# Kernel optimization log

Hardware: AMD Instinct MI355X
Metric: run time of the kernel (lower is better)

## Reference

```python
import jax, jax.numpy as jnp
import numpy as np

NUM_ANCHORS = 9  # 3 ratios * 3 sizes


def setup_inputs() -> dict:
    key = jax.random.key(0)
    k0, k1, k2, k3 = jax.random.split(key, 4)
    B, C, H, W = 4, 256, 200, 336
    resnet_features = jax.random.normal(k0, (B, C, H, W), dtype=jnp.float32)
    # 3x3 conv: C -> 512
    W1 = jax.random.normal(k1, (512, C, 3, 3), dtype=jnp.float32) * 0.02
    b1 = jnp.zeros((512,), dtype=jnp.float32)
    # 1x1 cls head: 512 -> 9*2
    Wc = jax.random.normal(k2, (NUM_ANCHORS * 2, 512), dtype=jnp.float32) * 0.02
    bc = jnp.zeros((NUM_ANCHORS * 2,), dtype=jnp.float32)
    # 1x1 bbox head: 512 -> 9*4
    Wb = jax.random.normal(k3, (NUM_ANCHORS * 4, 512), dtype=jnp.float32) * 0.02
    bb = jnp.zeros((NUM_ANCHORS * 4,), dtype=jnp.float32)
    return {"resnet_features": resnet_features, "W1": W1, "b1": b1,
            "Wc": Wc, "bc": bc, "Wb": Wb, "bb": bb}


def reference(resnet_features, W1, b1, Wc, bc, Wb, bb):
    B = resnet_features.shape[0]
    # conv3x3 + ReLU (padding=1 -> SAME)
    feat = jax.lax.conv_general_dilated(
        resnet_features, W1, window_strides=(1, 1), padding='SAME',
        dimension_numbers=('NCHW', 'OIHW', 'NCHW'))
    feat = jax.nn.relu(feat + b1[None, :, None, None])  # [B,512,H,W]
    # 1x1 conv heads as channel contractions
    cls = jnp.einsum('bchw,oc->bohw', feat, Wc) + bc[None, :, None, None]
    box = jnp.einsum('bchw,oc->bohw', feat, Wb) + bb[None, :, None, None]
    # permute(0,2,3,1).view(B,-1,2/4)
    anchor_cls_score = jnp.transpose(cls, (0, 2, 3, 1)).reshape(B, -1, 2)
    anchor_bboxdelta = jnp.transpose(box, (0, 2, 3, 1)).reshape(B, -1, 4)
    return anchor_cls_score, anchor_bboxdelta
```

## Files before the change

### kernel.cpp

```cpp
#include <hip/hip_runtime.h>
#include <hip/hip_bf16.h>
#include <stdint.h>

#define B_   4
#define C_   256
#define H_   200
#define W_   336
#define OC_  512
#define HP_  202
#define WP_  338
#define M_   (B_*H_*W_)
#define MTILES (M_/128)
#define OUT0_ (M_*18)
#define OUT_TOTAL_ (M_*54)

#define XP_ELEMS  ((size_t)B_*HP_*WP_*C_)
#define XP_BYTES  (XP_ELEMS*2)
#define W1T_ELEMS ((size_t)9*OC_*C_)
#define W1T_OFF   XP_BYTES
#define WHB_OFF   (W1T_OFF + W1T_ELEMS*2)

typedef unsigned short ushortT;
typedef __attribute__((ext_vector_type(8))) short bf16x8;
typedef __attribute__((ext_vector_type(4))) float f32x4;

static __device__ __forceinline__ ushortT f2bf(float x) {
    union { float f; uint32_t u; } v; v.f = x;
    uint32_t r = v.u + 0x7fff + ((v.u >> 16) & 1);
    return (ushortT)(r >> 16);
}

__global__ __launch_bounds__(256) void zero_halo(ushortT* __restrict__ Xp) {
    int i = blockIdx.x * 256 + threadIdx.x;
    if (i >= 4 * 1076 * 32) return;
    int pix = i >> 5, ch = (i & 31) * 8;
    int b = pix / 1076, r = pix % 1076;
    int h, w;
    if (r < 338)      { h = 0;   w = r; }
    else if (r < 676) { h = 201; w = r - 338; }
    else { r -= 676; h = 1 + (r >> 1); w = (r & 1) ? 337 : 0; }
    size_t dst = (((size_t)b*HP_ + h)*WP_ + w)*C_ + ch;
    *(uint4*)(Xp + dst) = make_uint4(0, 0, 0, 0);
}

__global__ __launch_bounds__(256) void pad_transpose(const float* __restrict__ X,
                                                     ushortT* __restrict__ Xp) {
    int bid = blockIdx.x;
    int wc = bid % 6; int bh = bid / 6;
    int h = bh % H_;  int b = bh / H_;
    int w0 = wc * 64;
    int t = threadIdx.x;
    __shared__ ushortT tile[64 * 65];

    for (int c0 = 0; c0 < C_; c0 += 64) {
        if (c0) __syncthreads();
        int col  = t & 63;
        int rowb = t >> 6;
        #pragma unroll
        for (int rr = 0; rr < 16; ++rr) {
            int row = rowb * 16 + rr;
            int w = w0 + col;
            float val = 0.f;
            if (w < W_)
                val = X[(((size_t)(b*C_ + c0 + row))*H_ + h)*W_ + w];
            tile[row*65 + col] = f2bf(val);
        }
        __syncthreads();
        int pixel = t >> 2;
        int csub  = (t & 3) * 16;
        int w = w0 + pixel;
        if (w < W_) {
            union { ushortT u[16]; uint4 q[2]; } vals;
            #pragma unroll
            for (int j = 0; j < 16; ++j)
                vals.u[j] = tile[(csub + j)*65 + pixel];
            size_t dst = (((size_t)b*HP_ + (h+1))*WP_ + (w+1))*C_ + c0 + csub;
            *(uint4*)(Xp + dst)     = vals.q[0];
            *(uint4*)(Xp + dst + 8) = vals.q[1];
        }
    }
}

__global__ __launch_bounds__(256) void prep_w1(const float* __restrict__ W1,
                                               ushortT* __restrict__ W1t) {
    int t = blockIdx.x * 256 + threadIdx.x;
    if (t >= OC_*C_) return;
    const float* src = W1 + (size_t)t * 9;
    #pragma unroll
    for (int rs = 0; rs < 9; ++rs)
        W1t[(size_t)rs*OC_*C_ + t] = f2bf(src[rs]);
}

__global__ __launch_bounds__(256) void prep_whb(const float* __restrict__ Wc,
                                                const float* __restrict__ Wb,
                                                ushortT* __restrict__ Whb) {
    int t = blockIdx.x * 256 + threadIdx.x;
    if (t >= 64*512) return;
    int o = t >> 9, oc = t & 511;
    float v = 0.f;
    if (o < 18) v = Wc[o*512 + oc];
    else if (o < 54) v = Wb[(o-18)*512 + oc];
    Whb[t] = f2bf(v);
}

__global__ __launch_bounds__(256) void init_out(const float* __restrict__ bc,
                                                const float* __restrict__ bb,
                                                float* __restrict__ out) {
    int i = blockIdx.x * 256 + threadIdx.x;
    if (i >= OUT_TOTAL_/4) return;
    int base = i * 4;
    float4 v;
    #pragma unroll
    for (int j = 0; j < 4; ++j) {
        int idx = base + j;
        float val = (idx < OUT0_) ? bc[idx % 18] : bb[(idx - OUT0_) % 36];
        (&v.x)[j] = val;
    }
    ((float4*)out)[i] = v;
}

#define FP_ 136

#define GRID_GROUPS ((MTILES + 7) / 8)
#define CONV_GRID   (GRID_GROUPS * 32)

__global__ __launch_bounds__(256, 4) void conv_rpn(
    const ushortT* __restrict__ Xp, const ushortT* __restrict__ W1t,
    const float* __restrict__ b1,  const ushortT* __restrict__ Whb,
    float* __restrict__ out)
{
    extern __shared__ ushortT smem[];
    ushortT* Asm = smem;
    ushortT* Bsm = smem + 128*64;
    ushortT* Fsm = smem;

    const int tid  = threadIdx.x;
    const int wave = tid >> 6;
    const int lane = tid & 63;
    const int col  = lane & 15;
    const int quad = lane >> 4;

    const int bidx   = blockIdx.x;
    const int grp    = bidx >> 5;
    const int within = bidx & 31;
    const int mtile  = grp * 8 + (within & 7);
    const int nblk   = within >> 3;
    if (mtile >= MTILES) return;
    const int oc0 = nblk << 7;

    const int r8     = lane >> 3;
    const int lchunk = ((lane & 7) ^ r8) * 8;

    size_t pixbase[4];
    #pragma unroll
    for (int i = 0; i < 4; ++i) {
        int m = mtile*128 + wave*32 + i*8 + r8;
        int b = m / (H_*W_);
        int rem = m % (H_*W_);
        int h = rem / W_;
        int w = rem % W_;
        pixbase[i] = (((size_t)b*HP_ + h)*WP_ + w)*C_ + lchunk;
    }
    const size_t bbase = ((size_t)(oc0 + wave*32 + r8))*C_ + lchunk;

    f32x4 acc[4][4] = {};
    const int wm = (wave & 1) * 64;
    const int wn = (wave >> 1) * 64;
    const int c7 = col & 7;

    for (int rs = 0; rs < 9; ++rs) {
        const int roff = ((rs/3)*WP_ + (rs%3)) * C_;
        const size_t wsrc = (size_t)rs*OC_*C_;
        for (int cs = 0; cs < C_; cs += 64) {
            __syncthreads();
            #pragma unroll
            for (int i = 0; i < 4; ++i) {
                const ushortT* g = Xp + pixbase[i] + roff + cs;
                ushortT* l = Asm + (wave*32 + i*8)*64;
                __builtin_amdgcn_global_load_lds(
                    (const __attribute__((address_space(1))) uint32_t*)g,
                    (__attribute__((address_space(3))) uint32_t*)l, 16, 0, 0);
            }
            #pragma unroll
            for (int i = 0; i < 4; ++i) {
                const ushortT* g = W1t + wsrc + bbase + (size_t)i*8*C_ + cs;
                ushortT* l = Bsm + (wave*32 + i*8)*64;
                __builtin_amdgcn_global_load_lds(
                    (const __attribute__((address_space(1))) uint32_t*)g,
                    (__attribute__((address_space(3))) uint32_t*)l, 16, 0, 0);
            }
            __syncthreads();

            #pragma unroll
            for (int kk = 0; kk < 2; ++kk) {
                const int pcA = ((kk*4 + quad) ^ c7) * 8;
                bf16x8 af[4], bfr[4];
                #pragma unroll
                for (int mt = 0; mt < 4; ++mt)
                    af[mt] = *(const bf16x8*)&Asm[(wm + mt*16 + col)*64 + pcA];
                #pragma unroll
                for (int nt = 0; nt < 4; ++nt)
                    bfr[nt] = *(const bf16x8*)&Bsm[(wn + nt*16 + col)*64 + pcA];
                #pragma unroll
                for (int mt = 0; mt < 4; ++mt)
                    #pragma unroll
                    for (int nt = 0; nt < 4; ++nt)
                        acc[mt][nt] = __builtin_amdgcn_mfma_f32_16x16x32_bf16(
                            af[mt], bfr[nt], acc[mt][nt], 0, 0, 0);
            }
        }
    }

    __syncthreads();
    float b1v[4];
    #pragma unroll
    for (int nt = 0; nt < 4; ++nt) b1v[nt] = b1[oc0 + wn + nt*16 + col];
    #pragma unroll
    for (int mt = 0; mt < 4; ++mt)
        #pragma unroll
        for (int nt = 0; nt < 4; ++nt)
            #pragma unroll
            for (int rg = 0; rg < 4; ++rg) {
                float v = acc[mt][nt][rg] + b1v[nt];
                v = fmaxf(v, 0.f);
                Fsm[(wm + mt*16 + quad*4 + rg)*FP_ + wn + nt*16 + col] = f2bf(v);
            }
    __syncthreads();

    f32x4 hacc[2][4] = {};
    #pragma unroll
    for (int ks = 0; ks < 4; ++ks) {
        bf16x8 ah[2];
        #pragma unroll
        for (int mt = 0; mt < 2; ++mt)
            ah[mt] = *(const bf16x8*)&Fsm[(wave*32 + mt*16 + col)*FP_ + ks*32 + quad*8];
        #pragma unroll
        for (int nt = 0; nt < 4; ++nt) {
            bf16x8 bh = *(const bf16x8*)&Whb[(nt*16 + col)*512 + oc0 + ks*32 + quad*8];
            #pragma unroll
            for (int mt = 0; mt < 2; ++mt)
                hacc[mt][nt] = __builtin_amdgcn_mfma_f32_16x16x32_bf16(
                    ah[mt], bh, hacc[mt][nt], 0, 0, 0);
        }
    }

    #pragma unroll
    for (int mt = 0; mt < 2; ++mt) {
        int mbase = mtile*128 + wave*32 + mt*16 + quad*4;
        #pragma unroll
        for (int nt = 0; nt < 4; ++nt) {
            int o = nt*16 + col;
            #pragma unroll
            for (int rg = 0; rg < 4; ++rg) {
                float v = hacc[mt][nt][rg];
                size_t p = (size_t)(mbase + rg);
                if (o < 18)      atomicAdd(out + p*18 + o, v);
                else if (o < 54) atomicAdd(out + OUT0_ + p*36 + (o - 18), v);
            }
        }
    }
}

extern "C" void kernel_launch(void* const* d_in, const int* in_sizes, int n_in,
                              void* d_out, int out_size, void* d_ws, size_t ws_size,
                              hipStream_t stream) {
    const float* X  = (const float*)d_in[0];
    const float* W1 = (const float*)d_in[1];
    const float* b1 = (const float*)d_in[2];
    const float* Wc = (const float*)d_in[3];
    const float* bc = (const float*)d_in[4];
    const float* Wb = (const float*)d_in[5];
    const float* bb = (const float*)d_in[6];
    float* out = (float*)d_out;

    ushortT* Xp  = (ushortT*)d_ws;
    ushortT* W1t = (ushortT*)((char*)d_ws + W1T_OFF);
    ushortT* Whb = (ushortT*)((char*)d_ws + WHB_OFF);

    zero_halo<<<(4*1076*32 + 255)/256, 256, 0, stream>>>(Xp);
    pad_transpose<<<B_*H_*6, 256, 0, stream>>>(X, Xp);
    prep_w1<<<(OC_*C_ + 255)/256, 256, 0, stream>>>(W1, W1t);
    prep_whb<<<(64*512 + 255)/256, 256, 0, stream>>>(Wc, Wb, Whb);
    init_out<<<(OUT_TOTAL_/4 + 255)/256, 256, 0, stream>>>(bc, bb, out);
    conv_rpn<<<CONV_GRID, 256, 128*FP_*sizeof(ushortT), stream>>>(
        Xp, W1t, b1, Whb, out);
}
```

Before: 1.143 ms.

## Compute full 512-channel tile per block with double-buffered LDS pipeline, drop atomics

Each block now handles a 128-pixel tile across all 512 output channels using 512 threads, so the head GEMM runs fully in-block. Output is written directly with bias instead of through an init kernel plus atomicAdd. The K loop is flattened into 36 stages with double-buffered async global-to-LDS loads overlapped with MFMA, and tiles are mapped to XCDs explicitly. This costs much more LDS (160KB) and more registers per thread, which limits occupancy.

```diff
diff --git a/kernel.cpp b/kernel.cpp
--- a/kernel.cpp
+++ b/kernel.cpp
@@ -103,160 +103,152 @@
     Whb[t] = f2bf(v);
 }
 
-__global__ __launch_bounds__(256) void init_out(const float* __restrict__ bc,
-                                                const float* __restrict__ bb,
-                                                float* __restrict__ out) {
-    int i = blockIdx.x * 256 + threadIdx.x;
-    if (i >= OUT_TOTAL_/4) return;
-    int base = i * 4;
-    float4 v;
-    #pragma unroll
-    for (int j = 0; j < 4; ++j) {
-        int idx = base + j;
-        float val = (idx < OUT0_) ? bc[idx % 18] : bb[(idx - OUT0_) % 36];
-        (&v.x)[j] = val;
-    }
-    ((float4*)out)[i] = v;
-}
-
-#define FP_ 136
-
-#define GRID_GROUPS ((MTILES + 7) / 8)
-#define CONV_GRID   (GRID_GROUPS * 32)
-
-__global__ __launch_bounds__(256, 4) void conv_rpn(
+#define CONV_GRID 2100
+
+__global__ __launch_bounds__(512, 2) void conv_rpn(
     const ushortT* __restrict__ Xp, const ushortT* __restrict__ W1t,
     const float* __restrict__ b1,  const ushortT* __restrict__ Whb,
+    const float* __restrict__ bc,  const float* __restrict__ bb,
     float* __restrict__ out)
 {
     extern __shared__ ushortT smem[];
-    ushortT* Asm = smem;
-    ushortT* Bsm = smem + 128*64;
-    ushortT* Fsm = smem;
 
     const int tid  = threadIdx.x;
     const int wave = tid >> 6;
     const int lane = tid & 63;
     const int col  = lane & 15;
     const int quad = lane >> 4;
-
-    const int bidx   = blockIdx.x;
-    const int grp    = bidx >> 5;
-    const int within = bidx & 31;
-    const int mtile  = grp * 8 + (within & 7);
-    const int nblk   = within >> 3;
-    if (mtile >= MTILES) return;
-    const int oc0 = nblk << 7;
+    const int c7   = col & 7;
+    const int wm   = (wave >> 2) * 64;
+    const int wn   = (wave & 3) * 128;
+
+    const int bid = blockIdx.x;
+    const int xcd = bid & 7, ib = bid >> 3;
+    const int mtile = (xcd < 4) ? (xcd*263 + ib) : (1052 + (xcd-4)*262 + ib);
 
     const int r8     = lane >> 3;
     const int lchunk = ((lane & 7) ^ r8) * 8;
 
-    size_t pixbase[4];
-    #pragma unroll
-    for (int i = 0; i < 4; ++i) {
-        int m = mtile*128 + wave*32 + i*8 + r8;
+    size_t pixA[2];
+    #pragma unroll
+    for (int i = 0; i < 2; ++i) {
+        int m = mtile*128 + wave*16 + i*8 + r8;
         int b = m / (H_*W_);
         int rem = m % (H_*W_);
-        int h = rem / W_;
-        int w = rem % W_;
-        pixbase[i] = (((size_t)b*HP_ + h)*WP_ + w)*C_ + lchunk;
-    }
-    const size_t bbase = ((size_t)(oc0 + wave*32 + r8))*C_ + lchunk;
-
-    f32x4 acc[4][4] = {};
-    const int wm = (wave & 1) * 64;
-    const int wn = (wave >> 1) * 64;
-    const int c7 = col & 7;
-
-    for (int rs = 0; rs < 9; ++rs) {
+        int hh = rem / W_;
+        int ww = rem % W_;
+        pixA[i] = (((size_t)b*HP_ + hh)*WP_ + ww)*C_ + lchunk;
+    }
+    const size_t bbase = ((size_t)(wave*64 + r8))*C_ + lchunk;
+
+    f32x4 acc[4][8] = {};
+
+    auto STAGE = [&](int t, int buf) {
+        const int rs = t >> 2;
+        const int cs = (t & 3) << 6;
         const int roff = ((rs/3)*WP_ + (rs%3)) * C_;
-        const size_t wsrc = (size_t)rs*OC_*C_;
-        for (int cs = 0; cs < C_; cs += 64) {
-            __syncthreads();
-            #pragma unroll
-            for (int i = 0; i < 4; ++i) {
-                const ushortT* g = Xp + pixbase[i] + roff + cs;
-                ushortT* l = Asm + (wave*32 + i*8)*64;
-                __builtin_amdgcn_global_load_lds(
-                    (const __attribute__((address_space(1))) uint32_t*)g,
-                    (__attribute__((address_space(3))) uint32_t*)l, 16, 0, 0);
+        const size_t wsrc = (size_t)rs*OC_*C_ + bbase + cs;
+        ushortT* Ab = smem + buf*8192  + (wave*16)*64;
+        ushortT* Bb = smem + 16384 + buf*32768 + (wave*64)*64;
+        #pragma unroll
+        for (int i = 0; i < 2; ++i)
+            __builtin_amdgcn_global_load_lds(
+                (const __attribute__((address_space(1))) uint32_t*)(Xp + pixA[i] + roff + cs),
+                (__attribute__((address_space(3))) uint32_t*)(Ab + i*8*64), 16, 0, 0);
+        #pragma unroll
+        for (int i = 0; i < 8; ++i)
+            __builtin_amdgcn_global_load_lds(
+                (const __attribute__((address_space(1))) uint32_t*)(W1t + wsrc + (size_t)i*8*C_),
+                (__attribute__((address_space(3))) uint32_t*)(Bb + i*8*64), 16, 0, 0);
+    };
+
+    STAGE(0, 0);
+
+    #pragma unroll 1
+    for (int t = 0; t < 36; ++t) {
+        const int cur = t & 1;
+        if (t < 35) {
+            STAGE(t + 1, cur ^ 1);
+            asm volatile("s_waitcnt vmcnt(10)" ::: "memory");
+        } else {
+            asm volatile("s_waitcnt vmcnt(0)" ::: "memory");
+        }
+        __builtin_amdgcn_sched_barrier(0);
+        __builtin_amdgcn_s_barrier();
+        __builtin_amdgcn_sched_barrier(0);
+
+        const ushortT* Al = smem + cur*8192;
+        const ushortT* Bl = smem + 16384 + cur*32768;
+        #pragma unroll
+        for (int kk = 0; kk < 2; ++kk) {
+            const int pc = ((kk*4 + quad) ^ c7) * 8;
+            bf16x8 af[4], bfr[8];
+            #pragma unroll
+            for (int mt = 0; mt < 4; ++mt)
+                af[mt] = *(const bf16x8*)&Al[(wm + mt*16 + col)*64 + pc];
+            #pragma unroll
+            for (int nt = 0; nt < 8; ++nt)
+                bfr[nt] = *(const bf16x8*)&Bl[(wn + nt*16 + col)*64 + pc];
+            __builtin_amdgcn_s_setprio(1);
+            #pragma unroll
+            for (int mt = 0; mt < 4; ++mt)
+                #pragma unroll
+                for (int nt = 0; nt < 8; ++nt)
+                    acc[mt][nt] = __builtin_amdgcn_mfma_f32_16x16x32_bf16(
+                        af[mt], bfr[nt], acc[mt][nt], 0, 0, 0);
+            __builtin_amdgcn_s_setprio(0);
+        }
+        asm volatile("s_waitcnt lgkmcnt(0)" ::: "memory");
+        __builtin_amdgcn_sched_barrier(0);
+        __builtin_amdgcn_s_barrier();
+        __builtin_amdgcn_sched_barrier(0);
+    }
+
+    ushortT* Fsm = smem;
+    float b1v[8];
+    #pragma unroll
+    for (int nt = 0; nt < 8; ++nt) b1v[nt] = b1[wn + nt*16 + col];
+    #pragma unroll
+    for (int mt = 0; mt < 4; ++mt)
+        #pragma unroll
+        for (int nt = 0; nt < 8; ++nt) {
+            const float bv = b1v[nt];
+            #pragma unroll
+            for (int rg = 0; rg < 4; ++rg) {
+                int row  = wm + mt*16 + quad*4 + rg;
+                int colc = wn + nt*16 + col;
+                float v = fmaxf(acc[mt][nt][rg] + bv, 0.f);
+                int pos = (((colc >> 3) ^ (row & 7)) << 3) | (colc & 7);
+                Fsm[row*512 + pos] = f2bf(v);
             }
-            #pragma unroll
-            for (int i = 0; i < 4; ++i) {
-                const ushortT* g = W1t + wsrc + bbase + (size_t)i*8*C_ + cs;
-                ushortT* l = Bsm + (wave*32 + i*8)*64;
-                __builtin_amdgcn_global_load_lds(
-                    (const __attribute__((address_space(1))) uint32_t*)g,
-                    (__attribute__((address_space(3))) uint32_t*)l, 16, 0, 0);
-            }
-            __syncthreads();
-
-            #pragma unroll
-            for (int kk = 0; kk < 2; ++kk) {
-                const int pcA = ((kk*4 + quad) ^ c7) * 8;
-                bf16x8 af[4], bfr[4];
-                #pragma unroll
-                for (int mt = 0; mt < 4; ++mt)
-                    af[mt] = *(const bf16x8*)&Asm[(wm + mt*16 + col)*64 + pcA];
-                #pragma unroll
-                for (int nt = 0; nt < 4; ++nt)
-                    bfr[nt] = *(const bf16x8*)&Bsm[(wn + nt*16 + col)*64 + pcA];
-                #pragma unroll
-                for (int mt = 0; mt < 4; ++mt)
-                    #pragma unroll
-                    for (int nt = 0; nt < 4; ++nt)
-                        acc[mt][nt] = __builtin_amdgcn_mfma_f32_16x16x32_bf16(
-                            af[mt], bfr[nt], acc[mt][nt], 0, 0, 0);
-            }
-        }
-    }
-
+        }
     __syncthreads();
-    float b1v[4];
-    #pragma unroll
-    for (int nt = 0; nt < 4; ++nt) b1v[nt] = b1[oc0 + wn + nt*16 + col];
-    #pragma unroll
-    for (int mt = 0; mt < 4; ++mt)
-        #pragma unroll
-        for (int nt = 0; nt < 4; ++nt)
-            #pragma unroll
-            for (int rg = 0; rg < 4; ++rg) {
-                float v = acc[mt][nt][rg] + b1v[nt];
-                v = fmaxf(v, 0.f);
-                Fsm[(wm + mt*16 + quad*4 + rg)*FP_ + wn + nt*16 + col] = f2bf(v);
-            }
-    __syncthreads();
-
-    f32x4 hacc[2][4] = {};
-    #pragma unroll
-    for (int ks = 0; ks < 4; ++ks) {
-        bf16x8 ah[2];
-        #pragma unroll
-        for (int mt = 0; mt < 2; ++mt)
-            ah[mt] = *(const bf16x8*)&Fsm[(wave*32 + mt*16 + col)*FP_ + ks*32 + quad*8];
+
+    f32x4 hacc[4] = {};
+    const int hrow = wave*16 + col;
+    const int h7   = col & 7;
+    const ushortT* Fr = Fsm + hrow*512;
+    #pragma unroll
+    for (int ks = 0; ks < 16; ++ks) {
+        bf16x8 ah = *(const bf16x8*)&Fr[((ks*4 + quad) ^ h7) << 3];
         #pragma unroll
         for (int nt = 0; nt < 4; ++nt) {
-            bf16x8 bh = *(const bf16x8*)&Whb[(nt*16 + col)*512 + oc0 + ks*32 + quad*8];
-            #pragma unroll
-            for (int mt = 0; mt < 2; ++mt)
-                hacc[mt][nt] = __builtin_amdgcn_mfma_f32_16x16x32_bf16(
-                    ah[mt], bh, hacc[mt][nt], 0, 0, 0);
-        }
-    }
-
-    #pragma unroll
-    for (int mt = 0; mt < 2; ++mt) {
-        int mbase = mtile*128 + wave*32 + mt*16 + quad*4;
-        #pragma unroll
-        for (int nt = 0; nt < 4; ++nt) {
-            int o = nt*16 + col;
-            #pragma unroll
-            for (int rg = 0; rg < 4; ++rg) {
-                float v = hacc[mt][nt][rg];
-                size_t p = (size_t)(mbase + rg);
-                if (o < 18)      atomicAdd(out + p*18 + o, v);
-                else if (o < 54) atomicAdd(out + OUT0_ + p*36 + (o - 18), v);
-            }
+            bf16x8 bh = *(const bf16x8*)&Whb[(nt*16 + col)*512 + ks*32 + quad*8];
+            hacc[nt] = __builtin_amdgcn_mfma_f32_16x16x32_bf16(
+                ah, bh, hacc[nt], 0, 0, 0);
+        }
+    }
+
+    #pragma unroll
+    for (int nt = 0; nt < 4; ++nt) {
+        int o = nt*16 + col;
+        float bias = (o < 18) ? bc[o] : (o < 54 ? bb[o - 18] : 0.f);
+        #pragma unroll
+        for (int rg = 0; rg < 4; ++rg) {
+            size_t p = (size_t)mtile*128 + wave*16 + quad*4 + rg;
+            float v = hacc[nt][rg] + bias;
+            if (o < 18)      out[p*18 + o] = v;
+            else if (o < 54) out[OUT0_ + p*36 + (o - 18)] = v;
         }
     }
 }
@@ -277,11 +269,16 @@
     ushortT* W1t = (ushortT*)((char*)d_ws + W1T_OFF);
     ushortT* Whb = (ushortT*)((char*)d_ws + WHB_OFF);
 
+    static bool attr_set = false;
+    if (!attr_set) {
+        hipFuncSetAttribute((const void*)conv_rpn,
+                            hipFuncAttributeMaxDynamicSharedMemorySize, 163840);
+        attr_set = true;
+    }
+
     zero_halo<<<(4*1076*32 + 255)/256, 256, 0, stream>>>(Xp);
     pad_transpose<<<B_*H_*6, 256, 0, stream>>>(X, Xp);
     prep_w1<<<(OC_*C_ + 255)/256, 256, 0, stream>>>(W1, W1t);
     prep_whb<<<(64*512 + 255)/256, 256, 0, stream>>>(Wc, Wb, Whb);
-    init_out<<<(OUT_TOTAL_/4 + 255)/256, 256, 0, stream>>>(bc, bb, out);
-    conv_rpn<<<CONV_GRID, 256, 128*FP_*sizeof(ushortT), stream>>>(
-        Xp, W1t, b1, Whb, out);
-}
+    conv_rpn<<<CONV_GRID, 512, 163840, stream>>>(Xp, W1t, b1, Whb, bc, bb, out);
+}
```

After: 1.150 ms. No clear change (+0.6%).

## Use 256x256 tiles with double-buffered LDS prefetch and XCD-aware block mapping

Applied to the files above, without the earlier changes.

The conv GEMM is retiled so each 512-thread block computes a 256-pixel by 256-channel tile. The block count drops to two per M tile, which raises data reuse per LDS load. Global-to-LDS loads for the next K step are split into four quarters and interleaved with the MFMA phases using two LDS buffers, explicit waitcnt/barriers, and s_setprio. Block IDs are remapped so neighbouring tiles land on the same XCD, and the head epilogue now reduces over 256 channels with a swizzled LDS layout. The cost is 128KB of LDS per block and lower occupancy, with more complex synchronisation.

```diff
diff --git a/kernel.cpp b/kernel.cpp
--- a/kernel.cpp
+++ b/kernel.cpp
@@ -10,7 +10,7 @@
 #define HP_  202
 #define WP_  338
 #define M_   (B_*H_*W_)
-#define MTILES (M_/128)
+#define MT256 (M_/256)
 #define OUT0_ (M_*18)
 #define OUT_TOTAL_ (M_*54)
 
@@ -119,124 +119,221 @@
     ((float4*)out)[i] = v;
 }
 
-#define FP_ 136
-
-#define GRID_GROUPS ((MTILES + 7) / 8)
-#define CONV_GRID   (GRID_GROUPS * 32)
-
-__global__ __launch_bounds__(256, 4) void conv_rpn(
+#define CONV_GRID 2100
+
+#define GLD(gsrc, ldst) __builtin_amdgcn_global_load_lds( \
+    (const __attribute__((address_space(1))) uint32_t*)(gsrc), \
+    (__attribute__((address_space(3))) uint32_t*)(ldst), 16, 0, 0)
+
+__global__ __launch_bounds__(512, 2) void conv_rpn(
     const ushortT* __restrict__ Xp, const ushortT* __restrict__ W1t,
     const float* __restrict__ b1,  const ushortT* __restrict__ Whb,
     float* __restrict__ out)
 {
     extern __shared__ ushortT smem[];
-    ushortT* Asm = smem;
-    ushortT* Bsm = smem + 128*64;
-    ushortT* Fsm = smem;
 
     const int tid  = threadIdx.x;
     const int wave = tid >> 6;
     const int lane = tid & 63;
     const int col  = lane & 15;
     const int quad = lane >> 4;
-
-    const int bidx   = blockIdx.x;
-    const int grp    = bidx >> 5;
-    const int within = bidx & 31;
-    const int mtile  = grp * 8 + (within & 7);
-    const int nblk   = within >> 3;
-    if (mtile >= MTILES) return;
-    const int oc0 = nblk << 7;
+    const int c7   = col & 7;
+    const int wm   = (wave >> 2) * 128;
+    const int wn64 = (wave & 3) * 64;
+
+    const int bid = blockIdx.x;
+    const int xcd = bid & 7, ib = bid >> 3;
+    const int seq = (xcd < 4) ? (xcd*263 + ib) : (1052 + (xcd-4)*262 + ib);
+    const int mtile = seq >> 1;
+    const int nh    = seq & 1;
 
     const int r8     = lane >> 3;
     const int lchunk = ((lane & 7) ^ r8) * 8;
 
-    size_t pixbase[4];
-    #pragma unroll
-    for (int i = 0; i < 4; ++i) {
-        int m = mtile*128 + wave*32 + i*8 + r8;
-        int b = m / (H_*W_);
-        int rem = m % (H_*W_);
-        int h = rem / W_;
-        int w = rem % W_;
-        pixbase[i] = (((size_t)b*HP_ + h)*WP_ + w)*C_ + lchunk;
-    }
-    const size_t bbase = ((size_t)(oc0 + wave*32 + r8))*C_ + lchunk;
-
-    f32x4 acc[4][4] = {};
-    const int wm = (wave & 1) * 64;
-    const int wn = (wave >> 1) * 64;
-    const int c7 = col & 7;
-
-    for (int rs = 0; rs < 9; ++rs) {
-        const int roff = ((rs/3)*WP_ + (rs%3)) * C_;
-        const size_t wsrc = (size_t)rs*OC_*C_;
-        for (int cs = 0; cs < C_; cs += 64) {
-            __syncthreads();
-            #pragma unroll
-            for (int i = 0; i < 4; ++i) {
-                const ushortT* g = Xp + pixbase[i] + roff + cs;
-                ushortT* l = Asm + (wave*32 + i*8)*64;
-                __builtin_amdgcn_global_load_lds(
-                    (const __attribute__((address_space(1))) uint32_t*)g,
-                    (__attribute__((address_space(3))) uint32_t*)l, 16, 0, 0);
+    size_t pixA[2][2];
+    #pragma unroll
+    for (int h = 0; h < 2; ++h)
+        #pragma unroll
+        for (int l = 0; l < 2; ++l) {
+            int m = mtile*256 + h*128 + wave*16 + l*8 + r8;
+            int b = m / (H_*W_);
+            int rem = m % (H_*W_);
+            int hh = rem / W_;
+            int ww = rem % W_;
+            pixA[h][l] = (((size_t)b*HP_ + hh)*WP_ + ww)*C_ + lchunk;
+        }
+    size_t bbase[2][2];
+    #pragma unroll
+    for (int h = 0; h < 2; ++h)
+        #pragma unroll
+        for (int l = 0; l < 2; ++l)
+            bbase[h][l] = ((size_t)(nh*256 + h*128 + wave*16 + l*8 + r8))*C_
+                          + lchunk;
+
+    f32x4 acc[2][4][4] = {};
+
+    auto STAGE_HALF = [&](int q, int buf, size_t aoffn, size_t woffn) {
+        if (q < 2) {
+            ushortT* dst = smem + buf*16384 + (q*128 + wave*16)*64;
+            GLD(Xp + pixA[q][0] + aoffn, dst);
+            GLD(Xp + pixA[q][1] + aoffn, dst + 8*64);
+        } else {
+            int h = q - 2;
+            ushortT* dst = smem + 32768 + buf*16384 + (h*128 + wave*16)*64;
+            GLD(W1t + woffn + bbase[h][0], dst);
+            GLD(W1t + woffn + bbase[h][1], dst + 8*64);
+        }
+    };
+
+    STAGE_HALF(0, 0, 0, 0);
+    STAGE_HALF(1, 0, 0, 0);
+    STAGE_HALF(2, 0, 0, 0);
+    STAGE_HALF(3, 0, 0, 0);
+
+    #pragma unroll 1
+    for (int t = 0; t < 36; ++t) {
+        const int cur = t & 1;
+        const ushortT* Al = smem + cur*16384;
+        const ushortT* Bl = smem + 32768 + cur*16384;
+        const bool pf = (t < 35);
+        size_t aoffn = 0, woffn = 0;
+        if (pf) {
+            int tn = t + 1;
+            int rsn = tn >> 2, csn = (tn & 3) << 6;
+            aoffn = (size_t)((rsn/3)*WP_ + (rsn%3))*C_ + csn;
+            woffn = (size_t)rsn*OC_*C_ + csn;
+        }
+        bf16x8 af[4], bfr[4];
+        const int pc0 = (quad ^ c7) * 8;
+        const int pc1 = ((4 + quad) ^ c7) * 8;
+
+        if (pf) {
+            STAGE_HALF(0, cur ^ 1, aoffn, woffn);
+            asm volatile("s_waitcnt vmcnt(2)" ::: "memory");
+        } else {
+            asm volatile("s_waitcnt vmcnt(0)" ::: "memory");
+        }
+        __builtin_amdgcn_sched_barrier(0);
+        __builtin_amdgcn_s_barrier();
+        __builtin_amdgcn_sched_barrier(0);
+        #pragma unroll
+        for (int mt = 0; mt < 4; ++mt)
+            af[mt] = *(const bf16x8*)&Al[(wm + mt*16 + col)*64 + pc0];
+        #pragma unroll
+        for (int nt = 0; nt < 4; ++nt)
+            bfr[nt] = *(const bf16x8*)&Bl[(wn64 + nt*16 + col)*64 + pc0];
+        asm volatile("s_waitcnt lgkmcnt(0)" ::: "memory");
+        __builtin_amdgcn_sched_barrier(0);
+        __builtin_amdgcn_s_setprio(1);
+        #pragma unroll
+        for (int mt = 0; mt < 4; ++mt)
+            #pragma unroll
+            for (int nt = 0; nt < 4; ++nt)
+                acc[0][mt][nt] = __builtin_amdgcn_mfma_f32_16x16x32_bf16(
+                    af[mt], bfr[nt], acc[0][mt][nt], 0, 0, 0);
+        __builtin_amdgcn_s_setprio(0);
+        __builtin_amdgcn_sched_barrier(0);
+        __builtin_amdgcn_s_barrier();
+
+        #pragma unroll
+        for (int mt = 0; mt < 4; ++mt)
+            af[mt] = *(const bf16x8*)&Al[(wm + 64 + mt*16 + col)*64 + pc0];
+        if (pf) STAGE_HALF(1, cur ^ 1, aoffn, woffn);
+        __builtin_amdgcn_s_barrier();
+        asm volatile("s_waitcnt lgkmcnt(0)" ::: "memory");
+        __builtin_amdgcn_sched_barrier(0);
+        __builtin_amdgcn_s_setprio(1);
+        #pragma unroll
+        for (int mt = 0; mt < 4; ++mt)
+            #pragma unroll
+            for (int nt = 0; nt < 4; ++nt)
+                acc[1][mt][nt] = __builtin_amdgcn_mfma_f32_16x16x32_bf16(
+                    af[mt], bfr[nt], acc[1][mt][nt], 0, 0, 0);
+        __builtin_amdgcn_s_setprio(0);
+        __builtin_amdgcn_sched_barrier(0);
+        __builtin_amdgcn_s_barrier();
+
+        #pragma unroll
+        for (int mt = 0; mt < 4; ++mt)
+            af[mt] = *(const bf16x8*)&Al[(wm + mt*16 + col)*64 + pc1];
+        #pragma unroll
+        for (int nt = 0; nt < 4; ++nt)
+            bfr[nt] = *(const bf16x8*)&Bl[(wn64 + nt*16 + col)*64 + pc1];
+        if (pf) STAGE_HALF(2, cur ^ 1, aoffn, woffn);
+        __builtin_amdgcn_s_barrier();
+        asm volatile("s_waitcnt lgkmcnt(0)" ::: "memory");
+        __builtin_amdgcn_sched_barrier(0);
+        __builtin_amdgcn_s_setprio(1);
+        #pragma unroll
+        for (int mt = 0; mt < 4; ++mt)
+            #pragma unroll
+            for (int nt = 0; nt < 4; ++nt)
+                acc[0][mt][nt] = __builtin_amdgcn_mfma_f32_16x16x32_bf16(
+                    af[mt], bfr[nt], acc[0][mt][nt], 0, 0, 0);
+        __builtin_amdgcn_s_setprio(0);
+        __builtin_amdgcn_sched_barrier(0);
+        __builtin_amdgcn_s_barrier();
+
+        #pragma unroll
+        for (int mt = 0; mt < 4; ++mt)
+            af[mt] = *(const bf16x8*)&Al[(wm + 64 + mt*16 + col)*64 + pc1];
+        if (pf) STAGE_HALF(3, cur ^ 1, aoffn, woffn);
+        __builtin_amdgcn_s_barrier();
+        asm volatile("s_waitcnt lgkmcnt(0)" ::: "memory");
+        __builtin_amdgcn_sched_barrier(0);
+        __builtin_amdgcn_s_setprio(1);
+        #pragma unroll
+        for (int mt = 0; mt < 4; ++mt)
+            #pragma unroll
+            for (int nt = 0; nt < 4; ++nt)
+                acc[1][mt][nt] = __builtin_amdgcn_mfma_f32_16x16x32_bf16(
+                    af[mt], bfr[nt], acc[1][mt][nt], 0, 0, 0);
+        __builtin_amdgcn_s_setprio(0);
+        __builtin_amdgcn_sched_barrier(0);
+        __builtin_amdgcn_s_barrier();
+    }
+
+    ushortT* Fsm = smem;
+    float b1v[4];
+    #pragma unroll
+    for (int mh = 0; mh < 2; ++mh) {
+        if (mh == 0) {
+            #pragma unroll
+            for (int nt = 0; nt < 4; ++nt)
+                b1v[nt] = b1[nh*256 + wn64 + nt*16 + col];
+        }
+        #pragma unroll
+        for (int mt = 0; mt < 4; ++mt)
+            #pragma unroll
+            for (int nt = 0; nt < 4; ++nt) {
+                const float bv = b1v[nt];
+                #pragma unroll
+                for (int rg = 0; rg < 4; ++rg) {
+                    int row  = wm + mh*64 + mt*16 + quad*4 + rg;
+                    int colc = wn64 + nt*16 + col;
+                    float v = fmaxf(acc[mh][mt][nt][rg] + bv, 0.f);
+                    int pos = (((colc >> 3) ^ (row & 7)) << 3) | (colc & 7);
+                    Fsm[row*256 + pos] = f2bf(v);
+                }
             }
-            #pragma unroll
-            for (int i = 0; i < 4; ++i) {
-                const ushortT* g = W1t + wsrc + bbase + (size_t)i*8*C_ + cs;
-                ushortT* l = Bsm + (wave*32 + i*8)*64;
-                __builtin_amdgcn_global_load_lds(
-                    (const __attribute__((address_space(1))) uint32_t*)g,
-                    (__attribute__((address_space(3))) uint32_t*)l, 16, 0, 0);
-            }
-            __syncthreads();
-
-            #pragma unroll
-            for (int kk = 0; kk < 2; ++kk) {
-                const int pcA = ((kk*4 + quad) ^ c7) * 8;
-                bf16x8 af[4], bfr[4];
-                #pragma unroll
-                for (int mt = 0; mt < 4; ++mt)
-                    af[mt] = *(const bf16x8*)&Asm[(wm + mt*16 + col)*64 + pcA];
-                #pragma unroll
-                for (int nt = 0; nt < 4; ++nt)
-                    bfr[nt] = *(const bf16x8*)&Bsm[(wn + nt*16 + col)*64 + pcA];
-                #pragma unroll
-                for (int mt = 0; mt < 4; ++mt)
-                    #pragma unroll
-                    for (int nt = 0; nt < 4; ++nt)
-                        acc[mt][nt] = __builtin_amdgcn_mfma_f32_16x16x32_bf16(
-                            af[mt], bfr[nt], acc[mt][nt], 0, 0, 0);
-            }
-        }
-    }
-
+    }
     __syncthreads();
-    float b1v[4];
-    #pragma unroll
-    for (int nt = 0; nt < 4; ++nt) b1v[nt] = b1[oc0 + wn + nt*16 + col];
-    #pragma unroll
-    for (int mt = 0; mt < 4; ++mt)
-        #pragma unroll
-        for (int nt = 0; nt < 4; ++nt)
-            #pragma unroll
-            for (int rg = 0; rg < 4; ++rg) {
-                float v = acc[mt][nt][rg] + b1v[nt];
-                v = fmaxf(v, 0.f);
-                Fsm[(wm + mt*16 + quad*4 + rg)*FP_ + wn + nt*16 + col] = f2bf(v);
-            }
-    __syncthreads();
 
     f32x4 hacc[2][4] = {};
-    #pragma unroll
-    for (int ks = 0; ks < 4; ++ks) {
+    const int h7 = col & 7;
+    #pragma unroll
+    for (int ks = 0; ks < 8; ++ks) {
         bf16x8 ah[2];
         #pragma unroll
-        for (int mt = 0; mt < 2; ++mt)
-            ah[mt] = *(const bf16x8*)&Fsm[(wave*32 + mt*16 + col)*FP_ + ks*32 + quad*8];
+        for (int mt = 0; mt < 2; ++mt) {
+            int hrow = wave*32 + mt*16 + col;
+            ah[mt] = *(const bf16x8*)&Fsm[hrow*256
+                        + (((ks*4 + quad) ^ h7) << 3)];
+        }
         #pragma unroll
         for (int nt = 0; nt < 4; ++nt) {
-            bf16x8 bh = *(const bf16x8*)&Whb[(nt*16 + col)*512 + oc0 + ks*32 + quad*8];
+            bf16x8 bh = *(const bf16x8*)&Whb[(nt*16 + col)*512
+                        + nh*256 + ks*32 + quad*8];
             #pragma unroll
             for (int mt = 0; mt < 2; ++mt)
                 hacc[mt][nt] = __builtin_amdgcn_mfma_f32_16x16x32_bf16(
@@ -246,7 +343,7 @@
 
     #pragma unroll
     for (int mt = 0; mt < 2; ++mt) {
-        int mbase = mtile*128 + wave*32 + mt*16 + quad*4;
+        int mbase = mtile*256 + wave*32 + mt*16 + quad*4;
         #pragma unroll
         for (int nt = 0; nt < 4; ++nt) {
             int o = nt*16 + col;
@@ -277,11 +374,17 @@
     ushortT* W1t = (ushortT*)((char*)d_ws + W1T_OFF);
     ushortT* Whb = (ushortT*)((char*)d_ws + WHB_OFF);
 
+    static bool attr_set = false;
+    if (!attr_set) {
+        hipFuncSetAttribute((const void*)conv_rpn,
+                            hipFuncAttributeMaxDynamicSharedMemorySize, 131072);
+        attr_set = true;
+    }
+
     zero_halo<<<(4*1076*32 + 255)/256, 256, 0, stream>>>(Xp);
     pad_transpose<<<B_*H_*6, 256, 0, stream>>>(X, Xp);
     prep_w1<<<(OC_*C_ + 255)/256, 256, 0, stream>>>(W1, W1t);
     prep_whb<<<(64*512 + 255)/256, 256, 0, stream>>>(Wc, Wb, Whb);
     init_out<<<(OUT_TOTAL_/4 + 255)/256, 256, 0, stream>>>(bc, bb, out);
-    conv_rpn<<<CONV_GRID, 256, 128*FP_*sizeof(ushortT), stream>>>(
-        Xp, W1t, b1, Whb, out);
-}
+    conv_rpn<<<CONV_GRID, 512, 131072, stream>>>(Xp, W1t, b1, Whb, out);
+}
```

Measured after the change: 1.168 ms. 1.02x slower.
